# Optimization experiments

Hardware: AMD Instinct MI355X
Metric: run time of the kernel (lower is better)

Reference implementation:

```python
import jax, jax.numpy as jnp
import numpy as np

N = 6144
FEAT = 512
HID = 256
KMAX = 50
KNN = 20
SPATIAL_DECAY = 50.0
THR = 0.1


def setup_inputs() -> dict:
    key = jax.random.key(0)
    ks = jax.random.split(key, 4)
    features = jax.random.normal(ks[0], (N, FEAT), dtype=jnp.float32)
    # spatial coordinates in a ~1000um slide, matches spatial_decay=50
    positions = jax.random.uniform(ks[1], (N, 2), dtype=jnp.float32) * 1000.0
    W1 = jax.random.normal(ks[2], (FEAT, HID), dtype=jnp.float32) * np.float32(1.0 / np.sqrt(FEAT))
    b1 = jnp.zeros((HID,), jnp.float32)
    W2 = jax.random.normal(ks[3], (HID, KMAX), dtype=jnp.float32) * np.float32(1.0 / np.sqrt(HID))
    b2 = jnp.zeros((KMAX,), jnp.float32)
    return {
        "features": features,
        "positions": positions,
        "lambda_weight": jnp.asarray(0.5, jnp.float32),
        "temperature": jnp.asarray(1.0, jnp.float32),
        "spatial_weight": jnp.asarray(1.0, jnp.float32),
        "W1": W1, "b1": b1, "W2": W2, "b2": b2,
    }


def reference(features, positions, lambda_weight, temperature, spatial_weight, W1, b1, W2, b2):
    n = features.shape[0]
    # --- LearnableAdjacency (Eq. 6) ---
    norm = jnp.maximum(jnp.linalg.norm(features, axis=1, keepdims=True), 1e-12)
    fn = features / norm
    sim = fn @ fn.T                                  # [N,N]
    p2 = jnp.sum(positions * positions, axis=1)
    d2 = jnp.maximum(p2[:, None] + p2[None, :] - 2.0 * (positions @ positions.T), 0.0)
    spatial_k = jnp.exp(-d2 / (2.0 * SPATIAL_DECAY ** 2))
    lam = jax.nn.sigmoid(lambda_weight)
    adj = jax.nn.sigmoid((lam * sim + (1.0 - lam) * spatial_k) * temperature)
    # row-wise top-k mask (scatter of ones)
    _, topk_idx = jax.lax.top_k(adj, KNN)
    mask = jnp.zeros_like(adj).at[jnp.arange(n)[:, None], topk_idx].set(1.0)
    adj = adj * mask

    # --- edge_index <=> binary adjacency (threshold 0.1) ---
    A_bin = (adj > THR).astype(adj.dtype)            # edge pattern used by GCN + loss

    # --- DifferentiablePooling: 2-layer GCN over the edge pattern ---
    # PyG GCNConv: add self-loops (diag already 1 -> becomes 2), deg from target (col) sums,
    # edge norm d_r^{-1/2} d_c^{-1/2}, aggregate at target: out = Mn^T (X W) + b
    M = A_bin + jnp.eye(n, dtype=adj.dtype)
    dinv = jax.lax.rsqrt(jnp.sum(M, axis=0))
    Mn = (dinv[:, None] * M) * dinv[None, :]
    h = jax.nn.relu(Mn.T @ (features @ W1) + b1)
    s = Mn.T @ (h @ W2) + b2
    K = max(5, min(KMAX, int(np.ceil(N / 50))))      # static: 50
    S = jax.nn.softmax(s[:, :K], axis=1)             # [N,K]

    # --- spatial loss (Eq. 9), vectorized segment form ---
    # sum over edges (i,j): (S_i . S_j) * ||p_i - p_j||^2  == sum(S * ((A_bin*d2) @ S))
    E = jnp.sum(A_bin)
    We = A_bin * d2
    L_spatial = spatial_weight * jnp.sum(S * (We @ S)) / E

    # --- coarsening (Eq. 8) ---
    X_t = S.T @ features                             # [K,FEAT]
    A_coarse = S.T @ (adj @ S)                       # [K,K]
    A_t = A_coarse * (A_coarse > THR).astype(A_coarse.dtype)
    return (S, X_t, A_t, L_spatial, lam)
```

## Files before the change

kernel.cpp:

```cpp
#include <hip/hip_runtime.h>
#include <hip/hip_bf16.h>
#include <math.h>

#define N_PTS   6144
#define FEAT    512
#define HID     256
#define KMAX    50
#define KNN     20
#define THR     0.1f
#define CW      1536
#define NCHUNK  4
#define CXC     64
#define NCHX    (N_PTS / CXC)

typedef unsigned short u16;
typedef __attribute__((ext_vector_type(8))) short bf16x8;
typedef __attribute__((ext_vector_type(8))) u16   u16x8;
typedef __attribute__((ext_vector_type(4))) float f32x4;

__device__ __forceinline__ u16 f2bf(float x) {
    union { float f; unsigned u; } a; a.f = x;
    unsigned r = (a.u + 0x7fffu + ((a.u >> 16) & 1u)) >> 16;
    return (u16)r;
}
__device__ __forceinline__ float bf2f(u16 h) {
    union { unsigned u; float f; } a; a.u = ((unsigned)h) << 16;
    return a.f;
}

__device__ __forceinline__ void gload16(const void* g, void* l) {
    __builtin_amdgcn_global_load_lds(
        (const __attribute__((address_space(1))) void*)g,
        (__attribute__((address_space(3))) void*)l, 16, 0, 0);
}

__global__ void init_kernel(int* __restrict__ indeg, int* __restrict__ fillc,
                            int* __restrict__ ec) {
    int t = blockIdx.x * blockDim.x + threadIdx.x;
    if (t < N_PTS) { indeg[t] = 0; fillc[t] = 0; }
    if (t == 0) { ec[0] = 0; }
}

__global__ __launch_bounds__(64) void normalize_kernel(const float* __restrict__ f,
                                                       u16* __restrict__ fnh,
                                                       u16* __restrict__ fnl,
                                                       u16* __restrict__ fh_,
                                                       u16* __restrict__ fl_) {
    int row = blockIdx.x, lane = threadIdx.x;
    const float4* fr = (const float4*)(f + (size_t)row * FEAT);
    float4 v0 = fr[lane * 2 + 0];
    float4 v1 = fr[lane * 2 + 1];
    float ss = v0.x * v0.x + v0.y * v0.y + v0.z * v0.z + v0.w * v0.w
             + v1.x * v1.x + v1.y * v1.y + v1.z * v1.z + v1.w * v1.w;
#pragma unroll
    for (int m = 1; m < 64; m <<= 1) ss += __shfl_xor(ss, m);
    float nrm = fmaxf(sqrtf(ss), 1e-12f);
    float r[8] = { v0.x, v0.y, v0.z, v0.w, v1.x, v1.y, v1.z, v1.w };
    u16x8 h, l, rh, rl;
#pragma unroll
    for (int q = 0; q < 8; q++) {
        float vn = r[q] / nrm;
        u16 hb = f2bf(vn);
        h[q] = hb; l[q] = f2bf(vn - bf2f(hb));
        u16 rb = f2bf(r[q]);
        rh[q] = rb; rl[q] = f2bf(r[q] - bf2f(rb));
    }
    size_t base = (size_t)row * FEAT + lane * 8;
    *(u16x8*)(fnh + base) = h;
    *(u16x8*)(fnl + base) = l;
    *(u16x8*)(fh_ + base) = rh;
    *(u16x8*)(fl_ + base) = rl;
}

__global__ void p2_kernel(const float* __restrict__ pos, float* __restrict__ p2) {
    int i = blockIdx.x * blockDim.x + threadIdx.x;
    if (i < N_PTS) {
        float x = pos[2 * i], y = pos[2 * i + 1];
        p2[i] = x * x + y * y;
    }
}

__global__ __launch_bounds__(256) void w1t_split_kernel(const float* __restrict__ W1,
                                                        u16* __restrict__ th,
                                                        u16* __restrict__ tl) {
    int n = blockIdx.x;
    for (int k = threadIdx.x; k < FEAT; k += 256) {
        float v = W1[(size_t)k * HID + n];
        u16 hb = f2bf(v);
        th[(size_t)n * FEAT + k] = hb;
        tl[(size_t)n * FEAT + k] = f2bf(v - bf2f(hb));
    }
}

__global__ __launch_bounds__(256) void w2t_split_kernel(const float* __restrict__ W2,
                                                        u16* __restrict__ th,
                                                        u16* __restrict__ tl) {
    int n = blockIdx.x, k = threadIdx.x;
    float v = (n < KMAX) ? W2[(size_t)k * KMAX + n] : 0.f;
    u16 hb = f2bf(v);
    th[(size_t)n * HID + k] = hb;
    tl[(size_t)n * HID + k] = f2bf(v - bf2f(hb));
}


__global__ __launch_bounds__(512) void gemm_adj_mfma_kernel(
    const u16* __restrict__ fnh, const u16* __restrict__ fnl,
    const float* __restrict__ pos, const float* __restrict__ p2,
    const float* __restrict__ lamw, const float* __restrict__ tempw,
    float* __restrict__ out, int c0) {
    __shared__ u16 Ah[128 * 32], Al[128 * 32], Bh[128 * 32], Bl[128 * 32];
    const int tid  = threadIdx.x;
    const int lane = tid & 63, wid = tid >> 6;
    const int wm = wid >> 2, wn = wid & 3;
    const int flat = blockIdx.y * gridDim.x + blockIdx.x;
    const int nwg  = gridDim.x * gridDim.y;
    const int swzb = (flat & 7) * (nwg >> 3) + (flat >> 3);
    const int bx = swzb % gridDim.x, by = swzb / gridDim.x;
    const int bm  = by * 128;
    const int bnl = bx * 128;
    const int bng = c0 + bnl;

    const int sbuf = wid >> 1, shalf = wid & 1;
    const u16* src = (sbuf & 1) ? fnl : fnh;
    u16* dst = (sbuf == 0) ? Ah : (sbuf == 1) ? Al : (sbuf == 2) ? Bh : Bl;
    const int grow = (sbuf >> 1) ? bng : bm;
    const u16* gbase = src + (size_t)(grow + shalf * 64 + (lane >> 2)) * FEAT
                     + (((lane & 3) ^ ((lane >> 3) & 3)) * 8);
    u16* ldst = dst + (shalf * 64) * 32;

    f32x4 acc[4][2];
#pragma unroll
    for (int m = 0; m < 4; m++)
#pragma unroll
        for (int n = 0; n < 2; n++) acc[m][n] = (f32x4){0.f, 0.f, 0.f, 0.f};

    const int fr = lane & 15;
    const int ks = lane >> 4;
    const int ksw = (ks ^ ((fr >> 1) & 3)) * 8;
    const int abase = (wm * 64 + fr) * 32 + ksw;
    const int bbase = (wn * 32 + fr) * 32 + ksw;

    for (int k0 = 0; k0 < FEAT; k0 += 32) {
#pragma unroll
        for (int i = 0; i < 4; i++)
            gload16(gbase + k0 + (size_t)i * 16 * FEAT, ldst + i * 512);
        __syncthreads();
        bf16x8 ahf[4], alf[4], bhf[2], blf[2];
#pragma unroll
        for (int m = 0; m < 4; m++) {
            ahf[m] = *(const bf16x8*)&Ah[abase + m * 16 * 32];
            alf[m] = *(const bf16x8*)&Al[abase + m * 16 * 32];
        }
#pragma unroll
        for (int n = 0; n < 2; n++) {
            bhf[n] = *(const bf16x8*)&Bh[bbase + n * 16 * 32];
            blf[n] = *(const bf16x8*)&Bl[bbase + n * 16 * 32];
        }
#pragma unroll
        for (int m = 0; m < 4; m++)
#pragma unroll
            for (int n = 0; n < 2; n++) {
                acc[m][n] = __builtin_amdgcn_mfma_f32_16x16x32_bf16(ahf[m], bhf[n], acc[m][n], 0, 0, 0);
                acc[m][n] = __builtin_amdgcn_mfma_f32_16x16x32_bf16(ahf[m], blf[n], acc[m][n], 0, 0, 0);
                acc[m][n] = __builtin_amdgcn_mfma_f32_16x16x32_bf16(alf[m], bhf[n], acc[m][n], 0, 0, 0);
            }
        __syncthreads();
    }

    float lam  = 1.f / (1.f + __expf(-lamw[0]));
    float temp = tempw[0];
    float p2c[2], pxc[2], pyc[2];
#pragma unroll
    for (int n = 0; n < 2; n++) {
        int cg = bng + wn * 32 + n * 16 + fr;
        p2c[n] = p2[cg]; pxc[n] = pos[2 * cg]; pyc[n] = pos[2 * cg + 1];
    }
#pragma unroll
    for (int m = 0; m < 4; m++) {
#pragma unroll
        for (int reg = 0; reg < 4; reg++) {
            int rrow = bm + wm * 64 + m * 16 + ks * 4 + reg;
            float p2r = p2[rrow], pxr = pos[2 * rrow], pyr = pos[2 * rrow + 1];
#pragma unroll
            for (int n = 0; n < 2; n++) {
                float sim = acc[m][n][reg];
                float d2 = fmaxf(p2r + p2c[n] - 2.f * (pxr * pxc[n] + pyr * pyc[n]), 0.f);
                float sk = __expf(-d2 * (1.f / 5000.f));
                float arg = (lam * sim + (1.f - lam) * sk) * temp;
                out[(size_t)rrow * CW + bnl + wn * 32 + n * 16 + fr] = 1.f / (1.f + __expf(-arg));
            }
        }
    }
}

__global__ __launch_bounds__(256) void gemm_z_kernel(
    const u16* __restrict__ xh, const u16* __restrict__ xl,
    const u16* __restrict__ w1th, const u16* __restrict__ w1tl,
    float* __restrict__ Z) {
    __shared__ u16 Ah[128 * 32], Al[128 * 32], Bh[128 * 32], Bl[128 * 32];
    const int tid  = threadIdx.x;
    const int lane = tid & 63, wid = tid >> 6;
    const int wm = wid >> 1, wn = wid & 1;
    const int flat = blockIdx.y * gridDim.x + blockIdx.x;
    const int nwg  = gridDim.x * gridDim.y;
    const int swzb = (flat & 7) * (nwg >> 3) + (flat >> 3);
    const int bm = (swzb / gridDim.x) * 128;
    const int bn = (swzb % gridDim.x) * 128;

    const u16* src; u16* dst; int grow;
    if      (wid == 0) { src = xh;   dst = Ah; grow = bm; }
    else if (wid == 1) { src = xl;   dst = Al; grow = bm; }
    else if (wid == 2) { src = w1th; dst = Bh; grow = bn; }
    else               { src = w1tl; dst = Bl; grow = bn; }
    const u16* gbase = src + (size_t)(grow + (lane >> 2)) * FEAT
                     + (((lane & 3) ^ ((lane >> 3) & 3)) * 8);

    f32x4 acc[4][4];
#pragma unroll
    for (int m = 0; m < 4; m++)
#pragma unroll
        for (int n = 0; n < 4; n++) acc[m][n] = (f32x4){0.f, 0.f, 0.f, 0.f};

    const int fr = lane & 15;
    const int ks = lane >> 4;
    const int ksw = (ks ^ ((fr >> 1) & 3)) * 8;
    const int abase = (wm * 64 + fr) * 32 + ksw;
    const int bbase = (wn * 64 + fr) * 32 + ksw;

    for (int k0 = 0; k0 < FEAT; k0 += 32) {
#pragma unroll
        for (int i = 0; i < 8; i++)
            gload16(gbase + k0 + (size_t)i * 16 * FEAT, dst + i * 512);
        __syncthreads();
        bf16x8 ahf[4], alf[4], bhf[4], blf[4];
#pragma unroll
        for (int m = 0; m < 4; m++) {
            ahf[m] = *(const bf16x8*)&Ah[abase + m * 16 * 32];
            alf[m] = *(const bf16x8*)&Al[abase + m * 16 * 32];
        }
#pragma unroll
        for (int n = 0; n < 4; n++) {
            bhf[n] = *(const bf16x8*)&Bh[bbase + n * 16 * 32];
            blf[n] = *(const bf16x8*)&Bl[bbase + n * 16 * 32];
        }
#pragma unroll
        for (int m = 0; m < 4; m++)
#pragma unroll
            for (int n = 0; n < 4; n++) {
                acc[m][n] = __builtin_amdgcn_mfma_f32_16x16x32_bf16(ahf[m], bhf[n], acc[m][n], 0, 0, 0);
                acc[m][n] = __builtin_amdgcn_mfma_f32_16x16x32_bf16(ahf[m], blf[n], acc[m][n], 0, 0, 0);
                acc[m][n] = __builtin_amdgcn_mfma_f32_16x16x32_bf16(alf[m], bhf[n], acc[m][n], 0, 0, 0);
            }
        __syncthreads();
    }
#pragma unroll
    for (int m = 0; m < 4; m++)
#pragma unroll
        for (int reg = 0; reg < 4; reg++) {
            int rrow = bm + wm * 64 + m * 16 + ks * 4 + reg;
#pragma unroll
            for (int n = 0; n < 4; n++)
                Z[(size_t)rrow * HID + bn + wn * 64 + n * 16 + fr] = acc[m][n][reg];
        }
}

__global__ __launch_bounds__(256) void gemm_y_kernel(
    const u16* __restrict__ hh, const u16* __restrict__ hl,
    const u16* __restrict__ w2th, const u16* __restrict__ w2tl,
    float* __restrict__ Y) {
    __shared__ u16 Ah[128 * 32], Al[128 * 32], Bh[64 * 32], Bl[64 * 32];
    const int tid  = threadIdx.x;
    const int lane = tid & 63, wid = tid >> 6;
    const int wm = wid >> 1, wn = wid & 1;
    const int bm = blockIdx.x * 128;

    const u16* src; u16* dst; int grow; int nld;
    if      (wid == 0) { src = hh;   dst = Ah; grow = bm; nld = 8; }
    else if (wid == 1) { src = hl;   dst = Al; grow = bm; nld = 8; }
    else if (wid == 2) { src = w2th; dst = Bh; grow = 0;  nld = 4; }
    else               { src = w2tl; dst = Bl; grow = 0;  nld = 4; }
    const u16* gbase = src + (size_t)(grow + (lane >> 2)) * HID
                     + (((lane & 3) ^ ((lane >> 3) & 3)) * 8);

    f32x4 acc[4][2];
#pragma unroll
    for (int m = 0; m < 4; m++)
#pragma unroll
        for (int n = 0; n < 2; n++) acc[m][n] = (f32x4){0.f, 0.f, 0.f, 0.f};

    const int fr = lane & 15;
    const int ks = lane >> 4;
    const int ksw = (ks ^ ((fr >> 1) & 3)) * 8;
    const int abase = (wm * 64 + fr) * 32 + ksw;
    const int bbase = (wn * 32 + fr) * 32 + ksw;

    for (int k0 = 0; k0 < HID; k0 += 32) {
        for (int i = 0; i < nld; i++)
            gload16(gbase + k0 + (size_t)i * 16 * HID, dst + i * 512);
        __syncthreads();
        bf16x8 ahf[4], alf[4], bhf[2], blf[2];
#pragma unroll
        for (int m = 0; m < 4; m++) {
            ahf[m] = *(const bf16x8*)&Ah[abase + m * 16 * 32];
            alf[m] = *(const bf16x8*)&Al[abase + m * 16 * 32];
        }
#pragma unroll
        for (int n = 0; n < 2; n++) {
            bhf[n] = *(const bf16x8*)&Bh[bbase + n * 16 * 32];
            blf[n] = *(const bf16x8*)&Bl[bbase + n * 16 * 32];
        }
#pragma unroll
        for (int m = 0; m < 4; m++)
#pragma unroll
            for (int n = 0; n < 2; n++) {
                acc[m][n] = __builtin_amdgcn_mfma_f32_16x16x32_bf16(ahf[m], bhf[n], acc[m][n], 0, 0, 0);
                acc[m][n] = __builtin_amdgcn_mfma_f32_16x16x32_bf16(ahf[m], blf[n], acc[m][n], 0, 0, 0);
                acc[m][n] = __builtin_amdgcn_mfma_f32_16x16x32_bf16(alf[m], bhf[n], acc[m][n], 0, 0, 0);
            }
        __syncthreads();
    }
#pragma unroll
    for (int m = 0; m < 4; m++)
#pragma unroll
        for (int reg = 0; reg < 4; reg++) {
            int rrow = bm + wm * 64 + m * 16 + ks * 4 + reg;
#pragma unroll
            for (int n = 0; n < 2; n++) {
                int col = wn * 32 + n * 16 + fr;
                if (col < KMAX) Y[(size_t)rrow * KMAX + col] = acc[m][n][reg];
            }
        }
}

__global__ __launch_bounds__(256) void topk_kernel(const float* __restrict__ chunk,
                                                   float* __restrict__ gval,
                                                   int* __restrict__ gidx, int c0) {
    const int lane = threadIdx.x & 63;
    const int row  = blockIdx.x * 4 + (threadIdx.x >> 6);
    float lv = -INFINITY; int li = -1;
    if (c0 > 0 && lane < KNN) {
        lv = gval[(size_t)row * KNN + lane];
        li = gidx[(size_t)row * KNN + lane];
    }
    float T = __shfl(lv, KNN - 1);
    const float4* rp = (const float4*)(chunk + (size_t)row * CW);
    float4 q[CW / 256];
#pragma unroll
    for (int b = 0; b < CW / 256; b++) q[b] = rp[lane + 64 * b];
#pragma unroll
    for (int b = 0; b < CW / 256; b++) {
        float vv[4] = { q[b].x, q[b].y, q[b].z, q[b].w };
        float bm4 = fmaxf(fmaxf(vv[0], vv[1]), fmaxf(vv[2], vv[3]));
#pragma unroll
        for (int msk = 1; msk < 64; msk <<= 1) bm4 = fmaxf(bm4, __shfl_xor(bm4, msk));
        if (bm4 <= T) continue;
#pragma unroll
        for (int e = 0; e < 4; e++) {
            unsigned long long bal = __ballot(vv[e] > T);
            while (bal) {
                int src = __ffsll((unsigned long long)bal) - 1;
                bal &= bal - 1;
                float cv = __shfl(vv[e], src);
                if (cv > T) {
                    int cc = c0 + 4 * (src + 64 * b) + e;
                    float up = __shfl_up(lv, 1);
                    int  upi = __shfl_up(li, 1);
                    if (lane == 0) up = INFINITY;
                    bool keep = lv > cv;
                    float nv = keep ? lv : (up > cv ? cv : up);
                    int  ni = keep ? li : (up > cv ? cc : upi);
                    lv = nv; li = ni;
                    T = __shfl(lv, KNN - 1);
                }
            }
        }
    }
    if (lane < KNN) {
        gval[(size_t)row * KNN + lane] = lv;
        gidx[(size_t)row * KNN + lane] = li;
    }
}

__global__ void degree_kernel(const float* __restrict__ gval, const int* __restrict__ gidx,
                              int* __restrict__ indeg, int* __restrict__ ec) {
    int e = blockIdx.x * blockDim.x + threadIdx.x;
    bool pass = gval[e] > THR;
    if (pass) atomicAdd(&indeg[gidx[e]], 1);
    unsigned long long b = __ballot(pass);
    if ((threadIdx.x & 63) == 0) atomicAdd(ec, (int)__popcll(b));
}

__global__ __launch_bounds__(1024) void scan_kernel(const int* __restrict__ indeg,
                                                    int* __restrict__ offs,
                                                    float* __restrict__ dinv) {
    __shared__ int part[1024];
    int tid = threadIdx.x;
    int d[6], loc[6], s = 0;
#pragma unroll
    for (int q = 0; q < 6; q++) { d[q] = indeg[tid * 6 + q]; loc[q] = s; s += d[q]; }
    part[tid] = s;
    __syncthreads();
    for (int off = 1; off < 1024; off <<= 1) {
        int v = (tid >= off) ? part[tid - off] : 0;
        __syncthreads();
        part[tid] += v;
        __syncthreads();
    }
    int pre = (tid > 0) ? part[tid - 1] : 0;
#pragma unroll
    for (int q = 0; q < 6; q++) {
        offs[tid * 6 + q] = pre + loc[q];
        dinv[tid * 6 + q] = 1.0f / sqrtf((float)(d[q] + 1));
    }
    if (tid == 1023) offs[N_PTS] = part[1023];
}

__global__ void fill_kernel(const float* __restrict__ gval, const int* __restrict__ gidx,
                            const int* __restrict__ offs, int* __restrict__ fillc,
                            int* __restrict__ csc) {
    int e = blockIdx.x * blockDim.x + threadIdx.x;
    if (gval[e] > THR) {
        int j = gidx[e];
        int pos = offs[j] + atomicAdd(&fillc[j], 1);
        csc[pos] = e / KNN;
    }
}

__global__ __launch_bounds__(256) void agg1_kernel(const float* __restrict__ Z,
                                                   const int* __restrict__ offs,
                                                   const int* __restrict__ csc,
                                                   const float* __restrict__ dinv,
                                                   const float* __restrict__ b1,
                                                   u16* __restrict__ hh,
                                                   u16* __restrict__ hl) {
    int j = blockIdx.x, f = threadIdx.x;
    float dj = dinv[j];
    float acc = dj * Z[(size_t)j * HID + f];
    int e = offs[j], e1 = offs[j + 1];
    for (; e + 4 <= e1; e += 4) {
        int i0 = csc[e], i1 = csc[e + 1], i2 = csc[e + 2], i3 = csc[e + 3];
        float w0 = dinv[i0], w1 = dinv[i1], w2 = dinv[i2], w3 = dinv[i3];
        float z0 = Z[(size_t)i0 * HID + f], z1 = Z[(size_t)i1 * HID + f];
        float z2 = Z[(size_t)i2 * HID + f], z3 = Z[(size_t)i3 * HID + f];
        acc = fmaf(w0, z0, acc); acc = fmaf(w1, z1, acc);
        acc = fmaf(w2, z2, acc); acc = fmaf(w3, z3, acc);
    }
    for (; e < e1; e++) {
        int i = csc[e];
        acc = fmaf(dinv[i], Z[(size_t)i * HID + f], acc);
    }
    float hv = fmaxf(acc * dj + b1[f], 0.f);
    u16 hb = f2bf(hv);
    hh[(size_t)j * HID + f] = hb;
    hl[(size_t)j * HID + f] = f2bf(hv - bf2f(hb));
}

__global__ __launch_bounds__(256) void agg2_softmax_kernel(const float* __restrict__ Y,
                                                           const int* __restrict__ offs,
                                                           const int* __restrict__ csc,
                                                           const float* __restrict__ dinv,
                                                           const float* __restrict__ b2,
                                                           float* __restrict__ S) {
    int c = threadIdx.x & 63;
    int j = blockIdx.x * 4 + (threadIdx.x >> 6);
    bool act = c < KMAX;
    float dj = dinv[j];
    float acc = act ? dj * Y[(size_t)j * KMAX + c] : 0.f;
    int e = offs[j], e1 = offs[j + 1];
    for (; e + 4 <= e1; e += 4) {
        int i0 = csc[e], i1 = csc[e + 1], i2 = csc[e + 2], i3 = csc[e + 3];
        float w0 = dinv[i0], w1 = dinv[i1], w2 = dinv[i2], w3 = dinv[i3];
        float y0 = act ? Y[(size_t)i0 * KMAX + c] : 0.f;
        float y1 = act ? Y[(size_t)i1 * KMAX + c] : 0.f;
        float y2 = act ? Y[(size_t)i2 * KMAX + c] : 0.f;
        float y3 = act ? Y[(size_t)i3 * KMAX + c] : 0.f;
        acc = fmaf(w0, y0, acc); acc = fmaf(w1, y1, acc);
        acc = fmaf(w2, y2, acc); acc = fmaf(w3, y3, acc);
    }
    for (; e < e1; e++) {
        int i = csc[e];
        if (act) acc = fmaf(dinv[i], Y[(size_t)i * KMAX + c], acc);
    }
    float s = act ? (acc * dj + b2[c]) : -INFINITY;
    float m = s;
#pragma unroll
    for (int msk = 1; msk < 64; msk <<= 1) m = fmaxf(m, __shfl_xor(m, msk));
    float ex = act ? expf(s - m) : 0.f;
    float tot = ex;
#pragma unroll
    for (int msk = 1; msk < 64; msk <<= 1) tot += __shfl_xor(tot, msk);
    if (act) S[(size_t)j * KMAX + c] = ex / tot;
}

__global__ __launch_bounds__(256) void rowops_kernel(const float* __restrict__ S,
                                                     const int* __restrict__ gidx,
                                                     const float* __restrict__ gval,
                                                     const float* __restrict__ pos,
                                                     const float* __restrict__ p2,
                                                     float* __restrict__ AS,
                                                     float* __restrict__ lossrow) {
    const int lane = threadIdx.x & 63;
    const int i = blockIdx.x * 4 + (threadIdx.x >> 6);
    const int c = lane;
    const bool act = c < KMAX;
    int jl = 0; float vl = 0.f, d2l = 0.f;
    if (lane < KNN) {
        jl = gidx[(size_t)i * KNN + lane];
        vl = gval[(size_t)i * KNN + lane];
        float pxi = pos[2 * i], pyi = pos[2 * i + 1], p2i = p2[i];
        d2l = fmaxf(p2i + p2[jl] - 2.f * (pxi * pos[2 * jl] + pyi * pos[2 * jl + 1]), 0.f);
    }
    float asum = 0.f, wsum = 0.f;
#pragma unroll
    for (int e = 0; e < KNN; e++) {
        int j = __shfl(jl, e);
        float v = __shfl(vl, e);
        float d2 = __shfl(d2l, e);
        float sv = act ? S[(size_t)j * KMAX + c] : 0.f;
        asum = fmaf(v, sv, asum);
        if (v > THR) wsum = fmaf(d2, sv, wsum);
    }
    if (act) AS[(size_t)i * KMAX + c] = asum;
    float li = act ? S[(size_t)i * KMAX + c] * wsum : 0.f;
#pragma unroll
    for (int m = 1; m < 64; m <<= 1) li += __shfl_xor(li, m);
    if (lane == 0) lossrow[i] = li;
}

__global__ __launch_bounds__(1024) void loss_reduce_kernel(const float* __restrict__ lossrow,
                                                           float* __restrict__ lossb) {
    int tid = threadIdx.x;
    float s = 0.f;
#pragma unroll
    for (int q = 0; q < 6; q++) s += lossrow[tid + 1024 * q];
#pragma unroll
    for (int m = 1; m < 64; m <<= 1) s += __shfl_xor(s, m);
    __shared__ float ws[16];
    if ((tid & 63) == 0) ws[tid >> 6] = s;
    __syncthreads();
    if (tid == 0) {
        float t = 0.f;
#pragma unroll
        for (int q = 0; q < 16; q++) t += ws[q];
        lossb[0] = t;
    }
}

__global__ __launch_bounds__(256) void coarseA_kernel(const float* __restrict__ S,
                                                      const float* __restrict__ AS,
                                                      float* __restrict__ Acp) {
    __shared__ float Ss[CXC][50];
    __shared__ float Bs[CXC][50];
    int tid = threadIdx.x;
    int ch = blockIdx.x;
    int i0 = ch * CXC;
    for (int idx = tid; idx < CXC * 50; idx += 256) {
        int r = idx / 50, c = idx % 50;
        Ss[r][c] = S[(size_t)(i0 + r) * KMAX + c];
        Bs[r][c] = AS[(size_t)(i0 + r) * KMAX + c];
    }
    __syncthreads();
    float acc[10];
    int ca[10], cb[10];
#pragma unroll
    for (int q = 0; q < 10; q++) {
        acc[q] = 0.f;
        int cell = tid + 256 * q;
        ca[q] = cell / 50; cb[q] = cell % 50;
    }
    for (int r = 0; r < CXC; r++) {
#pragma unroll
        for (int q = 0; q < 10; q++) {
            if (tid + 256 * q < 2500)
                acc[q] = fmaf(Ss[r][ca[q]], Bs[r][cb[q]], acc[q]);
        }
    }
#pragma unroll
    for (int q = 0; q < 10; q++) {
        int cell = tid + 256 * q;
        if (cell < 2500) Acp[(size_t)ch * 2500 + cell] = acc[q];
    }
}

__global__ __launch_bounds__(64) void coarseX_kernel(const float* __restrict__ S,
                                                     const float* __restrict__ X,
                                                     float* __restrict__ Xtp) {
    __shared__ float Ss[CXC][50];
    const int lane = threadIdx.x;
    const int ch = blockIdx.x >> 3;
    const int f = ((blockIdx.x & 7) << 6) + lane;
    const int i0 = ch * CXC;
    for (int idx = lane; idx < CXC * 50; idx += 64) {
        Ss[idx / 50][idx % 50] = S[(size_t)(i0 + idx / 50) * KMAX + idx % 50];
    }
    __syncthreads();
    float acc[50];
#pragma unroll
    for (int a = 0; a < 50; a++) acc[a] = 0.f;
    const float* xp = X + (size_t)i0 * FEAT + f;
#pragma unroll 4
    for (int r = 0; r < CXC; r++) {
        float xv = xp[(size_t)r * FEAT];
#pragma unroll
        for (int a = 0; a < 50; a++) acc[a] = fmaf(Ss[r][a], xv, acc[a]);
    }
#pragma unroll
    for (int a = 0; a < 50; a++)
        Xtp[((size_t)ch * KMAX + a) * FEAT + f] = acc[a];
}

__global__ __launch_bounds__(256) void reduceX_kernel(const float* __restrict__ Xtp,
                                                      float* __restrict__ Xt) {
    int cell = blockIdx.x * 256 + threadIdx.x;
    if (cell < KMAX * FEAT) {
        float s0 = 0.f, s1 = 0.f, s2 = 0.f, s3 = 0.f;
        for (int ch = 0; ch < NCHX; ch += 4) {
            s0 += Xtp[(size_t)ch * KMAX * FEAT + cell];
            s1 += Xtp[(size_t)(ch + 1) * KMAX * FEAT + cell];
            s2 += Xtp[(size_t)(ch + 2) * KMAX * FEAT + cell];
            s3 += Xtp[(size_t)(ch + 3) * KMAX * FEAT + cell];
        }
        Xt[cell] = (s0 + s1) + (s2 + s3);
    }
}

__global__ __launch_bounds__(256) void finalize_kernel(const float* __restrict__ Acp,
                                                       const float* __restrict__ loss,
                                                       const int* __restrict__ ec,
                                                       const float* __restrict__ sw,
                                                       const float* __restrict__ lamw,
                                                       float* __restrict__ out_At,
                                                       float* __restrict__ out_scalars) {
    int t = blockIdx.x * blockDim.x + threadIdx.x;
    if (t < KMAX * KMAX) {
        float s0 = 0.f, s1 = 0.f, s2 = 0.f, s3 = 0.f;
        for (int ch = 0; ch < NCHX; ch += 4) {
            s0 += Acp[(size_t)ch * 2500 + t];
            s1 += Acp[(size_t)(ch + 1) * 2500 + t];
            s2 += Acp[(size_t)(ch + 2) * 2500 + t];
            s3 += Acp[(size_t)(ch + 3) * 2500 + t];
        }
        float v = (s0 + s1) + (s2 + s3);
        out_At[t] = (v > THR) ? v : 0.f;
    }
    if (t == 0) {
        out_scalars[0] = sw[0] * loss[0] / (float)ec[0];
        out_scalars[1] = 1.f / (1.f + expf(-lamw[0]));
    }
}

extern "C" void kernel_launch(void* const* d_in, const int* in_sizes, int n_in,
                              void* d_out, int out_size, void* d_ws, size_t ws_size,
                              hipStream_t stream) {
    const float* features = (const float*)d_in[0];
    const float* positions = (const float*)d_in[1];
    const float* lambda_w  = (const float*)d_in[2];
    const float* temp_w    = (const float*)d_in[3];
    const float* spatial_w = (const float*)d_in[4];
    const float* W1 = (const float*)d_in[5];
    const float* b1 = (const float*)d_in[6];
    const float* W2 = (const float*)d_in[7];
    const float* b2 = (const float*)d_in[8];

    float* out = (float*)d_out;
    float* out_S  = out;
    float* out_Xt = out + (size_t)N_PTS * KMAX;
    float* out_At = out_Xt + KMAX * FEAT;
    float* out_sc = out_At + KMAX * KMAX;

    char* ws = (char*)d_ws;
    size_t off = 0;
    auto alloc = [&](size_t bytes) { size_t o = off; off = (off + bytes + 255) & ~(size_t)255; return o; };
    u16*   fnh     = (u16*)  (ws + alloc((size_t)N_PTS * FEAT * 2));
    u16*   fnl     = (u16*)  (ws + alloc((size_t)N_PTS * FEAT * 2));
    u16*   fh      = (u16*)  (ws + alloc((size_t)N_PTS * FEAT * 2));
    u16*   fl      = (u16*)  (ws + alloc((size_t)N_PTS * FEAT * 2));
    float* p2      = (float*)(ws + alloc((size_t)N_PTS * 4));
    float* adjchnk = (float*)(ws + alloc((size_t)N_PTS * CW * 4));
    float* gval    = (float*)(ws + alloc((size_t)N_PTS * KNN * 4));
    int*   gidx    = (int*)  (ws + alloc((size_t)N_PTS * KNN * 4));
    int*   indeg   = (int*)  (ws + alloc((size_t)N_PTS * 4));
    int*   fillc   = (int*)  (ws + alloc((size_t)N_PTS * 4));
    int*   offs    = (int*)  (ws + alloc((size_t)(N_PTS + 1) * 4));
    float* dinv    = (float*)(ws + alloc((size_t)N_PTS * 4));
    int*   csc     = (int*)  (ws + alloc((size_t)N_PTS * KNN * 4));
    u16*   w1th    = (u16*)  (ws + alloc((size_t)HID * FEAT * 2));
    u16*   w1tl    = (u16*)  (ws + alloc((size_t)HID * FEAT * 2));
    u16*   w2th    = (u16*)  (ws + alloc((size_t)64 * HID * 2));
    u16*   w2tl    = (u16*)  (ws + alloc((size_t)64 * HID * 2));
    float* lossrow = (float*)(ws + alloc((size_t)N_PTS * 4));
    float* lossb   = (float*)(ws + alloc(4));
    int*   ecnt    = (int*)  (ws + alloc(4));

    char* ov = (char*)adjchnk;
    float* Z   = (float*)(ov);
    u16*   hh  = (u16*)  (ov + 7 * 1024 * 1024);
    u16*   hl  = (u16*)  (ov + 11 * 1024 * 1024);
    float* Y   = (float*)(ov + 15 * 1024 * 1024);
    float* AS  = (float*)(ov + 17 * 1024 * 1024);
    float* Xtp = (float*)(ov + 19 * 1024 * 1024);
    float* Acp = (float*)(ov + 30 * 1024 * 1024);

    init_kernel<<<(N_PTS + 255) / 256, 256, 0, stream>>>(indeg, fillc, ecnt);
    normalize_kernel<<<N_PTS, 64, 0, stream>>>(features, fnh, fnl, fh, fl);
    p2_kernel<<<(N_PTS + 255) / 256, 256, 0, stream>>>(positions, p2);
    w1t_split_kernel<<<HID, 256, 0, stream>>>(W1, w1th, w1tl);
    w2t_split_kernel<<<64, 256, 0, stream>>>(W2, w2th, w2tl);
    for (int c = 0; c < NCHUNK; c++) {
        gemm_adj_mfma_kernel<<<dim3(CW / 128, N_PTS / 128), 512, 0, stream>>>(
            fnh, fnl, positions, p2, lambda_w, temp_w, adjchnk, c * CW);
        topk_kernel<<<N_PTS / 4, 256, 0, stream>>>(adjchnk, gval, gidx, c * CW);
    }
    degree_kernel<<<(N_PTS * KNN) / 256, 256, 0, stream>>>(gval, gidx, indeg, ecnt);
    scan_kernel<<<1, 1024, 0, stream>>>(indeg, offs, dinv);
    fill_kernel<<<(N_PTS * KNN) / 256, 256, 0, stream>>>(gval, gidx, offs, fillc, csc);
    gemm_z_kernel<<<dim3(HID / 128, N_PTS / 128), 256, 0, stream>>>(fh, fl, w1th, w1tl, Z);
    agg1_kernel<<<N_PTS, HID, 0, stream>>>(Z, offs, csc, dinv, b1, hh, hl);
    gemm_y_kernel<<<N_PTS / 128, 256, 0, stream>>>(hh, hl, w2th, w2tl, Y);
    agg2_softmax_kernel<<<N_PTS / 4, 256, 0, stream>>>(Y, offs, csc, dinv, b2, out_S);
    rowops_kernel<<<N_PTS / 4, 256, 0, stream>>>(out_S, gidx, gval, positions, p2, AS, lossrow);
    loss_reduce_kernel<<<1, 1024, 0, stream>>>(lossrow, lossb);
    coarseA_kernel<<<NCHX, 256, 0, stream>>>(out_S, AS, Acp);
    coarseX_kernel<<<NCHX * 8, 64, 0, stream>>>(out_S, features, Xtp);
    reduceX_kernel<<<(KMAX * FEAT + 255) / 256, 256, 0, stream>>>(Xtp, out_Xt);
    finalize_kernel<<<(KMAX * KMAX + 255) / 256, 256, 0, stream>>>(Acp, lossb, ecnt, spatial_w, lambda_w, out_At, out_sc);
}
```

Before: 493.9 us.

## Split top-k row scan across two wavefronts and merge partial lists

Each adjacency row chunk is now scanned by two wavefronts, each over half the columns and each keeping its own running top-20 list in a new 40-wide workspace. On the last chunk the two lists are merged through shared memory. The ballot now tests the per-lane max of four values instead of doing a wave-wide max reduction followed by four ballots. This doubles parallelism in the serial insertion loop, at the cost of more insertions (two independent thresholds) and a merge step.

```diff
diff --git a/kernel.cpp b/kernel.cpp
--- a/kernel.cpp
+++ b/kernel.cpp
@@ -333,36 +333,40 @@
 }
 
 __global__ __launch_bounds__(256) void topk_kernel(const float* __restrict__ chunk,
+                                                   float* __restrict__ gval2,
+                                                   int* __restrict__ gidx2,
                                                    float* __restrict__ gval,
-                                                   int* __restrict__ gidx, int c0) {
-    const int lane = threadIdx.x & 63;
-    const int row  = blockIdx.x * 4 + (threadIdx.x >> 6);
+                                                   int* __restrict__ gidx,
+                                                   int c0, int last) {
+    const int lane = threadIdx.x & 63, wid = threadIdx.x >> 6;
+    const int rib  = wid >> 1;
+    const int row  = blockIdx.x * 2 + rib;
+    const int half = wid & 1;
     float lv = -INFINITY; int li = -1;
     if (c0 > 0 && lane < KNN) {
-        lv = gval[(size_t)row * KNN + lane];
-        li = gidx[(size_t)row * KNN + lane];
+        lv = gval2[(size_t)row * 40 + half * KNN + lane];
+        li = gidx2[(size_t)row * 40 + half * KNN + lane];
     }
     float T = __shfl(lv, KNN - 1);
-    const float4* rp = (const float4*)(chunk + (size_t)row * CW);
-    float4 q[CW / 256];
-#pragma unroll
-    for (int b = 0; b < CW / 256; b++) q[b] = rp[lane + 64 * b];
-#pragma unroll
-    for (int b = 0; b < CW / 256; b++) {
+
+    const float4* rp = (const float4*)(chunk + (size_t)row * CW + half * (CW / 2));
+    float4 q[CW / 512];
+#pragma unroll
+    for (int b = 0; b < CW / 512; b++) q[b] = rp[lane + 64 * b];
+
+#pragma unroll
+    for (int b = 0; b < CW / 512; b++) {
         float vv[4] = { q[b].x, q[b].y, q[b].z, q[b].w };
-        float bm4 = fmaxf(fmaxf(vv[0], vv[1]), fmaxf(vv[2], vv[3]));
-#pragma unroll
-        for (int msk = 1; msk < 64; msk <<= 1) bm4 = fmaxf(bm4, __shfl_xor(bm4, msk));
-        if (bm4 <= T) continue;
-#pragma unroll
-        for (int e = 0; e < 4; e++) {
-            unsigned long long bal = __ballot(vv[e] > T);
-            while (bal) {
-                int src = __ffsll((unsigned long long)bal) - 1;
-                bal &= bal - 1;
+        float mx4 = fmaxf(fmaxf(vv[0], vv[1]), fmaxf(vv[2], vv[3]));
+        unsigned long long bal = __ballot(mx4 > T);
+        while (bal) {
+            int src = __ffsll((unsigned long long)bal) - 1;
+            bal &= bal - 1;
+#pragma unroll
+            for (int e = 0; e < 4; e++) {
                 float cv = __shfl(vv[e], src);
                 if (cv > T) {
-                    int cc = c0 + 4 * (src + 64 * b) + e;
+                    int cc = c0 + half * (CW / 2) + 4 * (src + 64 * b) + e;
                     float up = __shfl_up(lv, 1);
                     int  upi = __shfl_up(li, 1);
                     if (lane == 0) up = INFINITY;
@@ -375,9 +379,42 @@
             }
         }
     }
-    if (lane < KNN) {
-        gval[(size_t)row * KNN + lane] = lv;
-        gidx[(size_t)row * KNN + lane] = li;
+
+    if (last) {
+        __shared__ float sv[2][KNN];
+        __shared__ int   si[2][KNN];
+        if (half == 1 && lane < KNN) { sv[rib][lane] = lv; si[rib][lane] = li; }
+        __syncthreads();
+        if (half == 0) {
+            float bv = (lane < KNN) ? sv[rib][lane] : -INFINITY;
+            int   bi = (lane < KNN) ? si[rib][lane] : -1;
+            unsigned long long bal = __ballot(bv > T);
+            while (bal) {
+                int src = __ffsll((unsigned long long)bal) - 1;
+                bal &= bal - 1;
+                float cv = __shfl(bv, src);
+                if (cv > T) {
+                    int cc = __shfl(bi, src);
+                    float up = __shfl_up(lv, 1);
+                    int  upi = __shfl_up(li, 1);
+                    if (lane == 0) up = INFINITY;
+                    bool keep = lv > cv;
+                    float nv = keep ? lv : (up > cv ? cv : up);
+                    int  ni = keep ? li : (up > cv ? cc : upi);
+                    lv = nv; li = ni;
+                    T = __shfl(lv, KNN - 1);
+                }
+            }
+            if (lane < KNN) {
+                gval[(size_t)row * KNN + lane] = lv;
+                gidx[(size_t)row * KNN + lane] = li;
+            }
+        }
+    } else {
+        if (lane < KNN) {
+            gval2[(size_t)row * 40 + half * KNN + lane] = lv;
+            gidx2[(size_t)row * 40 + half * KNN + lane] = li;
+        }
     }
 }
 
@@ -679,6 +716,8 @@
     float* adjchnk = (float*)(ws + alloc((size_t)N_PTS * CW * 4));
     float* gval    = (float*)(ws + alloc((size_t)N_PTS * KNN * 4));
     int*   gidx    = (int*)  (ws + alloc((size_t)N_PTS * KNN * 4));
+    float* gval2   = (float*)(ws + alloc((size_t)N_PTS * 40 * 4));
+    int*   gidx2   = (int*)  (ws + alloc((size_t)N_PTS * 40 * 4));
     int*   indeg   = (int*)  (ws + alloc((size_t)N_PTS * 4));
     int*   fillc   = (int*)  (ws + alloc((size_t)N_PTS * 4));
     int*   offs    = (int*)  (ws + alloc((size_t)(N_PTS + 1) * 4));
@@ -709,7 +748,8 @@
     for (int c = 0; c < NCHUNK; c++) {
         gemm_adj_mfma_kernel<<<dim3(CW / 128, N_PTS / 128), 512, 0, stream>>>(
             fnh, fnl, positions, p2, lambda_w, temp_w, adjchnk, c * CW);
-        topk_kernel<<<N_PTS / 4, 256, 0, stream>>>(adjchnk, gval, gidx, c * CW);
+        topk_kernel<<<N_PTS / 2, 256, 0, stream>>>(adjchnk, gval2, gidx2, gval, gidx,
+                                                   c * CW, c == NCHUNK - 1);
     }
     degree_kernel<<<(N_PTS * KNN) / 256, 256, 0, stream>>>(gval, gidx, indeg, ecnt);
     scan_kernel<<<1, 1024, 0, stream>>>(indeg, offs, dinv);
```

Measured after the change: 564.2 us. 14.2% more time.

## Emit per-row tile maxima from adjacency GEMM and skip tiles in top-k

Applied to the files above, without the earlier changes.

The adjacency GEMM epilogue now reduces each row's maximum over every 128-column tile and writes it to a small rtmax buffer. The top-k kernel ranks the 12 tiles by that maximum, visits them in descending order, and stops once a tile's maximum cannot beat the current 20th value. This avoids reading most of the 1536-column chunk row from global memory. The cost is extra shuffles, a shared-memory reduction and a barrier in the GEMM epilogue, plus serialized per-tile loads in top-k that no longer batch the whole row up front.

```diff
diff --git a/kernel.cpp b/kernel.cpp
--- a/kernel.cpp
+++ b/kernel.cpp
@@ -10,6 +10,7 @@
 #define THR     0.1f
 #define CW      1536
 #define NCHUNK  4
+#define NTILE   12
 #define CXC     64
 #define NCHX    (N_PTS / CXC)
 
@@ -107,8 +108,9 @@
     const u16* __restrict__ fnh, const u16* __restrict__ fnl,
     const float* __restrict__ pos, const float* __restrict__ p2,
     const float* __restrict__ lamw, const float* __restrict__ tempw,
-    float* __restrict__ out, int c0) {
+    float* __restrict__ out, float* __restrict__ rtmax, int c0) {
     __shared__ u16 Ah[128 * 32], Al[128 * 32], Bh[128 * 32], Bl[128 * 32];
+    __shared__ float rmxs[128][4];
     const int tid  = threadIdx.x;
     const int lane = tid & 63, wid = tid >> 6;
     const int wm = wid >> 2, wn = wid & 3;
@@ -181,15 +183,27 @@
         for (int reg = 0; reg < 4; reg++) {
             int rrow = bm + wm * 64 + m * 16 + ks * 4 + reg;
             float p2r = p2[rrow], pxr = pos[2 * rrow], pyr = pos[2 * rrow + 1];
+            float mx = -INFINITY;
 #pragma unroll
             for (int n = 0; n < 2; n++) {
                 float sim = acc[m][n][reg];
                 float d2 = fmaxf(p2r + p2c[n] - 2.f * (pxr * pxc[n] + pyr * pyc[n]), 0.f);
                 float sk = __expf(-d2 * (1.f / 5000.f));
                 float arg = (lam * sim + (1.f - lam) * sk) * temp;
-                out[(size_t)rrow * CW + bnl + wn * 32 + n * 16 + fr] = 1.f / (1.f + __expf(-arg));
+                float o = 1.f / (1.f + __expf(-arg));
+                out[(size_t)rrow * CW + bnl + wn * 32 + n * 16 + fr] = o;
+                mx = fmaxf(mx, o);
             }
-        }
+#pragma unroll
+            for (int msk = 1; msk < 16; msk <<= 1) mx = fmaxf(mx, __shfl_xor(mx, msk));
+            if (fr == 0) rmxs[wm * 64 + m * 16 + ks * 4 + reg][wn] = mx;
+        }
+    }
+    __syncthreads();
+    if (tid < 128) {
+        float v = fmaxf(fmaxf(rmxs[tid][0], rmxs[tid][1]),
+                        fmaxf(rmxs[tid][2], rmxs[tid][3]));
+        rtmax[(size_t)(bm + tid) * NTILE + bx] = v;
     }
 }
 
@@ -333,6 +347,7 @@
 }
 
 __global__ __launch_bounds__(256) void topk_kernel(const float* __restrict__ chunk,
+                                                   const float* __restrict__ rtmax,
                                                    float* __restrict__ gval,
                                                    int* __restrict__ gidx, int c0) {
     const int lane = threadIdx.x & 63;
@@ -343,26 +358,32 @@
         li = gidx[(size_t)row * KNN + lane];
     }
     float T = __shfl(lv, KNN - 1);
-    const float4* rp = (const float4*)(chunk + (size_t)row * CW);
-    float4 q[CW / 256];
-#pragma unroll
-    for (int b = 0; b < CW / 256; b++) q[b] = rp[lane + 64 * b];
-#pragma unroll
-    for (int b = 0; b < CW / 256; b++) {
-        float vv[4] = { q[b].x, q[b].y, q[b].z, q[b].w };
-        float bm4 = fmaxf(fmaxf(vv[0], vv[1]), fmaxf(vv[2], vv[3]));
-#pragma unroll
-        for (int msk = 1; msk < 64; msk <<= 1) bm4 = fmaxf(bm4, __shfl_xor(bm4, msk));
-        if (bm4 <= T) continue;
-#pragma unroll
-        for (int e = 0; e < 4; e++) {
-            unsigned long long bal = __ballot(vv[e] > T);
-            while (bal) {
-                int src = __ffsll((unsigned long long)bal) - 1;
-                bal &= bal - 1;
-                float cv = __shfl(vv[e], src);
+    float tml = (lane < NTILE) ? rtmax[(size_t)row * NTILE + lane] : -INFINITY;
+    int rank = 0;
+#pragma unroll
+    for (int j = 0; j < NTILE; j++) {
+        float oj = __shfl(tml, j);
+        if (lane < NTILE && (oj > tml || (oj == tml && j < lane))) rank++;
+    }
+    const float2* rp = (const float2*)(chunk + (size_t)row * CW);
+    for (int t = 0; t < NTILE; t++) {
+        int srcl = __ffsll((unsigned long long)__ballot(lane < NTILE && rank == t)) - 1;
+        float tmt = __shfl(tml, srcl);
+        if (tmt <= T) break;
+        int tile = srcl;
+        float2 v2 = rp[tile * 64 + lane];
+        float mx2 = fmaxf(v2.x, v2.y);
+        unsigned long long bal = __ballot(mx2 > T);
+        while (bal) {
+            int src = __ffsll((unsigned long long)bal) - 1;
+            bal &= bal - 1;
+            float c0v = __shfl(v2.x, src);
+            float c1v = __shfl(v2.y, src);
+#pragma unroll
+            for (int e = 0; e < 2; e++) {
+                float cv = e ? c1v : c0v;
                 if (cv > T) {
-                    int cc = c0 + 4 * (src + 64 * b) + e;
+                    int cc = c0 + tile * 128 + 2 * src + e;
                     float up = __shfl_up(lv, 1);
                     int  upi = __shfl_up(li, 1);
                     if (lane == 0) up = INFINITY;
@@ -677,6 +698,7 @@
     u16*   fl      = (u16*)  (ws + alloc((size_t)N_PTS * FEAT * 2));
     float* p2      = (float*)(ws + alloc((size_t)N_PTS * 4));
     float* adjchnk = (float*)(ws + alloc((size_t)N_PTS * CW * 4));
+    float* rtmax   = (float*)(ws + alloc((size_t)N_PTS * NTILE * 4));
     float* gval    = (float*)(ws + alloc((size_t)N_PTS * KNN * 4));
     int*   gidx    = (int*)  (ws + alloc((size_t)N_PTS * KNN * 4));
     int*   indeg   = (int*)  (ws + alloc((size_t)N_PTS * 4));
@@ -707,9 +729,9 @@
     w1t_split_kernel<<<HID, 256, 0, stream>>>(W1, w1th, w1tl);
     w2t_split_kernel<<<64, 256, 0, stream>>>(W2, w2th, w2tl);
     for (int c = 0; c < NCHUNK; c++) {
-        gemm_adj_mfma_kernel<<<dim3(CW / 128, N_PTS / 128), 512, 0, stream>>>(
-            fnh, fnl, positions, p2, lambda_w, temp_w, adjchnk, c * CW);
-        topk_kernel<<<N_PTS / 4, 256, 0, stream>>>(adjchnk, gval, gidx, c * CW);
+        gemm_adj_mfma_kernel<<<dim3(NTILE, N_PTS / 128), 512, 0, stream>>>(
+            fnh, fnl, positions, p2, lambda_w, temp_w, adjchnk, rtmax, c * CW);
+        topk_kernel<<<N_PTS / 4, 256, 0, stream>>>(adjchnk, rtmax, gval, gidx, c * CW);
     }
     degree_kernel<<<(N_PTS * KNN) / 256, 256, 0, stream>>>(gval, gidx, indeg, ecnt);
     scan_kernel<<<1, 1024, 0, stream>>>(indeg, offs, dinv);
```

Result: no change. 500.3 us (+1.3%).
